# Kernel tuning notes

Hardware: AMD Instinct MI355X
Metric: run time of the kernel (lower is better)

The kernel has to match this reference:

```python
import jax, jax.numpy as jnp
import numpy as np

B, S, D = 2, 2048, 2048
H, KVH, HD = 16, 4, 128
GROUPS = H // KVH
SCALE = HD ** -0.5


def rotate_half(x):
    half = x.shape[-1] // 2
    return jnp.concatenate((-x[..., half:], x[..., :half]), axis=-1)


def apply_rope(q, k, cos, sin):
    # q,k: [B,S,H,HD]; cos,sin: [S,HD//2] -> repeat_interleave(2) -> [S,HD]
    cos = jnp.repeat(cos, 2, axis=-1)[None, :, None, :]
    sin = jnp.repeat(sin, 2, axis=-1)[None, :, None, :]
    return q * cos + rotate_half(q) * sin, k * cos + rotate_half(k) * sin


def setup_inputs() -> dict:
    key = jax.random.key(0)
    ks = jax.random.split(key, 8)
    inp = {
        'x': jax.random.normal(ks[0], (B, S, D), dtype=jnp.float32),
        'cos': jnp.cos(jnp.arange(S, dtype=jnp.float32)[:, None] * (1.0 / (10000.0 ** (jnp.arange(HD // 2, dtype=jnp.float32) / (HD // 2))))[None, :].reshape(1, HD // 2)),
        'sin': None,
        'mask': jnp.tril(jnp.ones((S, S), dtype=bool))[None, None, :, :],
        'Wq': jax.random.normal(ks[1], (D, H * HD), dtype=jnp.float32) * (D ** -0.5),
        'Wk': jax.random.normal(ks[2], (D, KVH * HD), dtype=jnp.float32) * (D ** -0.5),
        'Wv': jax.random.normal(ks[3], (D, KVH * HD), dtype=jnp.float32) * (D ** -0.5),
        'Wo': jax.random.normal(ks[4], (H * HD, D), dtype=jnp.float32) * ((H * HD) ** -0.5),
    }
    inv_freq = 1.0 / (10000.0 ** (jnp.arange(0, HD // 2, dtype=jnp.float32) / (HD // 2)))
    freqs = jnp.arange(S, dtype=jnp.float32)[:, None] * inv_freq[None, :]  # [S, HD//2]
    inp['cos'] = jnp.cos(freqs)
    inp['sin'] = jnp.sin(freqs)
    return inp


def reference(x, cos, sin, mask, Wq, Wk, Wv, Wo):
    b, s, _ = x.shape
    q = (x @ Wq).reshape(b, s, H, HD)    # [B,S,H,HD]
    k = (x @ Wk).reshape(b, s, KVH, HD)  # [B,S,KVH,HD]
    v = (x @ Wv).reshape(b, s, KVH, HD)
    q, k = apply_rope(q, k, cos, sin)
    q = q.transpose(0, 2, 1, 3)  # [B,H,S,HD]
    k = k.transpose(0, 2, 1, 3)  # [B,KVH,S,HD]
    v = v.transpose(0, 2, 1, 3)
    k = jnp.repeat(k, GROUPS, axis=1)  # [B,H,S,HD]
    v = jnp.repeat(v, GROUPS, axis=1)
    scores = jnp.einsum('bhqd,bhkd->bhqk', q, k) * SCALE
    scores = jnp.where(mask, scores, -jnp.inf)
    attn = jax.nn.softmax(scores, axis=-1)
    out = jnp.einsum('bhqk,bhkd->bhqd', attn, v)
    out = out.transpose(0, 2, 1, 3).reshape(b, s, H * HD)
    return out @ Wo
```

## Files before the change

kernel.cpp:

```cpp
#include <hip/hip_runtime.h>
#include <hip/hip_bf16.h>
#include <cstdint>
#include <type_traits>

typedef __attribute__((ext_vector_type(8))) short short8;
typedef __attribute__((ext_vector_type(4))) float floatx4;

constexpr int S_LEN = 2048;
constexpr float ATTN_SCALE = 0.08838834764831845f;
constexpr float LOG2E = 1.4426950408889634f;
constexpr float CP = ATTN_SCALE * LOG2E;

__device__ __forceinline__ void gl_lds16(const void* gp, void* lp) {
  __builtin_amdgcn_global_load_lds(
      (__attribute__((address_space(1))) void*)(uintptr_t)gp,
      (__attribute__((address_space(3))) void*)lp,
      16, 0, 0);
}

__device__ __forceinline__ float rowmax16(float x) {
  union { float f; int i; } a, b;
  a.f = x;
  b.i = __builtin_amdgcn_update_dpp(0, a.i, 0x121, 0xF, 0xF, true);
  x = fmaxf(x, b.f); a.f = x;
  b.i = __builtin_amdgcn_update_dpp(0, a.i, 0x122, 0xF, 0xF, true);
  x = fmaxf(x, b.f); a.f = x;
  b.i = __builtin_amdgcn_update_dpp(0, a.i, 0x124, 0xF, 0xF, true);
  x = fmaxf(x, b.f); a.f = x;
  b.i = __builtin_amdgcn_update_dpp(0, a.i, 0x128, 0xF, 0xF, true);
  return fmaxf(x, b.f);
}

__device__ __forceinline__ void rope8(short8 x0, short8 x1, const float* ca,
                                      const float* sa, const float* cb,
                                      const float* sb, short8& y0, short8& y1) {
#pragma unroll
  for (int e = 0; e < 8; ++e) {
    union { short s; __hip_bfloat16 h; } u0, u1, w0, w1;
    u0.s = x0[e]; u1.s = x1[e];
    float f0 = __bfloat162float(u0.h), f1 = __bfloat162float(u1.h);
    int j = e >> 1;
    w0.h = __float2bfloat16(f0 * ca[j] - f1 * sa[j]);
    w1.h = __float2bfloat16(f1 * cb[j] + f0 * sb[j]);
    y0[e] = w0.s; y1[e] = w1.s;
  }
}

__device__ __forceinline__ void tr32(const float* __restrict__ src,
                                     __hip_bfloat16* __restrict__ dst,
                                     int blk, int nblk_x, int N, int tid,
                                     float (*tile)[33]) {
  int n0 = (blk % nblk_x) * 32, k0 = (blk / nblk_x) * 32;
  int tx = tid & 31, ty = tid >> 5;
#pragma unroll
  for (int i = ty; i < 32; i += 8)
    tile[i][tx] = src[(size_t)(k0 + i) * N + n0 + tx];
  __syncthreads();
#pragma unroll
  for (int i = ty; i < 32; i += 8)
    dst[(size_t)(n0 + i) * 2048 + k0 + tx] = __float2bfloat16(tile[tx][i]);
}

__global__ void prep_kernel(const float* __restrict__ x,
                            const float* __restrict__ Wq,
                            const float* __restrict__ Wk,
                            const float* __restrict__ Wv,
                            const float* __restrict__ Wo,
                            __hip_bfloat16* __restrict__ xb,
                            __hip_bfloat16* __restrict__ wqkvt,
                            __hip_bfloat16* __restrict__ wot) {
  __shared__ float tile[32][33];
  int bx = blockIdx.x, tid = threadIdx.x;
  if (bx < 8192) {
    int i = bx * 256 + tid;
    float4 f = reinterpret_cast<const float4*>(x)[i];
    union { unsigned long long u64; __hip_bfloat16 h[4]; } u;
    u.h[0] = __float2bfloat16(f.x);
    u.h[1] = __float2bfloat16(f.y);
    u.h[2] = __float2bfloat16(f.z);
    u.h[3] = __float2bfloat16(f.w);
    reinterpret_cast<unsigned long long*>(xb)[i] = u.u64;
  } else if (bx < 12288) {
    tr32(Wq, wqkvt, bx - 8192, 64, 2048, tid, tile);
  } else if (bx < 13312) {
    tr32(Wk, wqkvt + 2048 * 2048, bx - 12288, 16, 512, tid, tile);
  } else if (bx < 14336) {
    tr32(Wv, wqkvt + 2560 * 2048, bx - 13312, 16, 512, tid, tile);
  } else {
    tr32(Wo, wot, bx - 14336, 64, 2048, tid, tile);
  }
}

__device__ __forceinline__ void gemm256_core(
    const __hip_bfloat16* __restrict__ Ab,
    const __hip_bfloat16* __restrict__ Bb,
    const int K, __hip_bfloat16* lds, floatx4 (&acc)[8][4]) {
  const int tid = threadIdx.x;
  const int wave = tid >> 6, lane = tid & 63;
  const int quad = lane >> 4, l15 = lane & 15;
  const int wm = wave >> 2, wn = wave & 3;
  const int nt = K >> 6;
  const int u2 = wave * 2;

  auto stA = [&](int tt, int h) {
    __hip_bfloat16* dst = lds + (tt & 1) * 32768;
    const int k0 = tt << 6;
#pragma unroll
    for (int j = 0; j < 2; ++j) {
      const int kc = (u2 + j) >> 1, rb = (u2 + j) & 1;
      gl_lds16(Ab + (size_t)(h * 128 + rb * 64 + lane) * K + k0 + kc * 8,
               dst + (kc * 256 + h * 128 + rb * 64) * 8);
    }
  };
  auto stB = [&](int tt, int h) {
    __hip_bfloat16* dst = lds + (tt & 1) * 32768 + 16384;
    const int k0 = tt << 6;
#pragma unroll
    for (int j = 0; j < 2; ++j) {
      const int kc = (u2 + j) >> 1, rb = (u2 + j) & 1;
      gl_lds16(Bb + (size_t)(h * 128 + rb * 64 + lane) * K + k0 + kc * 8,
               dst + (kc * 256 + h * 128 + rb * 64) * 8);
    }
  };

  stA(0, 0); stA(0, 1); stB(0, 0); stB(0, 1);
  if (nt > 1) { stB(1, 0); stB(1, 1); }
  asm volatile("s_waitcnt vmcnt(4)" ::: "memory");
  __builtin_amdgcn_s_barrier();

  const int abase = (quad * 256 + wm * 128 + l15) * 8;
  const int bbase = (quad * 256 + wn * 64 + l15) * 8;

#pragma unroll 2
  for (int t = 0; t < nt; ++t) {
    const __hip_bfloat16* Al = lds + (t & 1) * 32768;
    const __hip_bfloat16* Bl = Al + 16384;
    short8 b[2][4];
#pragma unroll
    for (int q = 0; q < 4; ++q) {
      short8 a[2][2];
#pragma unroll
      for (int kk = 0; kk < 2; ++kk) {
        if (q == 0) {
#pragma unroll
          for (int ni = 0; ni < 4; ++ni)
            b[kk][ni] = *(const short8*)&Bl[kk * 8192 + bbase + ni * 128];
        }
#pragma unroll
        for (int mi = 0; mi < 2; ++mi)
          a[kk][mi] = *(const short8*)&Al[kk * 8192 + abase + (2 * q + mi) * 128];
      }
      if (q == 0)      { if (t + 1 < nt) stA(t + 1, 0); }
      else if (q == 1) { if (t + 1 < nt) stA(t + 1, 1); }
      else if (q == 2) { if (t + 2 < nt) stB(t + 2, 0); }
      else             { if (t + 2 < nt) stB(t + 2, 1); }
      __builtin_amdgcn_s_barrier();
      asm volatile("s_waitcnt lgkmcnt(0)" ::: "memory");
      __builtin_amdgcn_sched_barrier(0);
      __builtin_amdgcn_s_setprio(1);
#pragma unroll
      for (int kk = 0; kk < 2; ++kk)
#pragma unroll
        for (int mi = 0; mi < 2; ++mi)
#pragma unroll
          for (int ni = 0; ni < 4; ++ni)
            acc[2 * q + mi][ni] = __builtin_amdgcn_mfma_f32_16x16x32_bf16(
                a[kk][mi], b[kk][ni], acc[2 * q + mi][ni], 0, 0, 0);
      __builtin_amdgcn_s_setprio(0);
      if (q == 3) {
        if (t + 2 < nt) asm volatile("s_waitcnt vmcnt(4)" ::: "memory");
        else            asm volatile("s_waitcnt vmcnt(0)" ::: "memory");
      }
      __builtin_amdgcn_s_barrier();
    }
  }
  asm volatile("" ::: "memory");
}

__global__ __launch_bounds__(512, 2) void qkv_gemm_kernel(
    const __hip_bfloat16* __restrict__ A,
    const __hip_bfloat16* __restrict__ Bt,
    __hip_bfloat16* __restrict__ qbuf,
    __hip_bfloat16* __restrict__ kbuf,
    __hip_bfloat16* __restrict__ vbuf,
    const float* __restrict__ cosb,
    const float* __restrict__ sinb) {
  constexpr int K = 2048;
  __shared__ __align__(16) __hip_bfloat16 lds[65536];
  const int tid = threadIdx.x;
  const int m0 = blockIdx.y * 256, n0 = blockIdx.x * 256;

  floatx4 acc[8][4] = {};
  gemm256_core(A + (size_t)m0 * K, Bt + (size_t)n0 * K, K, lds, acc);

  const int wave = tid >> 6, lane = tid & 63;
  const int quad = lane >> 4, l15 = lane & 15;
  const int wm = wave >> 2, wn = wave & 3;
  const bool isv = (n0 >= 2560);
  short* lds2 = (short*)lds;
#pragma unroll
  for (int mi = 0; mi < 8; ++mi)
#pragma unroll
    for (int ni = 0; ni < 4; ++ni)
#pragma unroll
      for (int r = 0; r < 4; ++r) {
        int row = wm * 128 + mi * 16 + quad * 4 + r;
        int col = wn * 64 + ni * 16 + l15;
        union { short s; __hip_bfloat16 h; } u;
        u.h = __float2bfloat16(acc[mi][ni][r]);
        if (isv) lds2[col * 256 + row] = u.s;
        else     lds2[row * 256 + col] = u.s;
      }
  __syncthreads();

  const int c16 = tid & 15, hh = c16 >> 3, c8 = c16 & 7;
  const int rid = tid >> 4, d0 = c8 * 8;
  if (n0 < 2048) {
#pragma unroll
    for (int j = 0; j < 8; ++j) {
      int rr = rid + 32 * j;
      int rowg = m0 + rr;
      int s = rowg & (S_LEN - 1);
      float ca[4], sa[4], cb[4], sb[4];
      *(float4*)ca = *(const float4*)&cosb[s * 64 + c8 * 4];
      *(float4*)sa = *(const float4*)&sinb[s * 64 + c8 * 4];
      *(float4*)cb = *(const float4*)&cosb[s * 64 + 32 + c8 * 4];
      *(float4*)sb = *(const float4*)&sinb[s * 64 + 32 + c8 * 4];
      short8 x0 = *(const short8*)&lds2[rr * 256 + hh * 128 + d0];
      short8 x1 = *(const short8*)&lds2[rr * 256 + hh * 128 + 64 + d0];
      short8 y0, y1;
      rope8(x0, x1, ca, sa, cb, sb, y0, y1);
      *(short8*)(qbuf + (size_t)rowg * 2048 + n0 + hh * 128 + d0) = y0;
      *(short8*)(qbuf + (size_t)rowg * 2048 + n0 + hh * 128 + 64 + d0) = y1;
    }
  } else if (!isv) {
    const int kvh = ((n0 - 2048) >> 7) + hh;
#pragma unroll
    for (int j = 0; j < 8; ++j) {
      int rr = rid + 32 * j;
      int rowg = m0 + rr;
      int s = rowg & (S_LEN - 1), bb = rowg >> 11;
      int kv = s & 63;
      size_t tb = ((size_t)(bb * 4 + kvh) * 32 + (s >> 6)) * 8192;
      float ca[4], sa[4], cb[4], sb[4];
      *(float4*)ca = *(const float4*)&cosb[s * 64 + c8 * 4];
      *(float4*)sa = *(const float4*)&sinb[s * 64 + c8 * 4];
      *(float4*)cb = *(const float4*)&cosb[s * 64 + 32 + c8 * 4];
      *(float4*)sb = *(const float4*)&sinb[s * 64 + 32 + c8 * 4];
      short8 x0 = *(const short8*)&lds2[rr * 256 + hh * 128 + d0];
      short8 x1 = *(const short8*)&lds2[rr * 256 + hh * 128 + 64 + d0];
      short8 y0, y1;
      rope8(x0, x1, ca, sa, cb, sb, y0, y1);
      *(short8*)(kbuf + tb + (size_t)c8 * 512 + kv * 8) = y0;
      *(short8*)(kbuf + tb + (size_t)(8 + c8) * 512 + kv * 8) = y1;
    }
  } else {
    const int kvh = ((n0 - 2560) >> 7) + hh;
    const int bb = m0 >> 11;
    const int kt0 = (m0 & (S_LEN - 1)) >> 6;
    const int kv0 = c8 * 8;
#pragma unroll
    for (int j = 0; j < 4; ++j) {
      int d = rid + 32 * j;
      int cxor = (d & 7) << 3;
#pragma unroll
      for (int half = 0; half < 4; ++half) {
        short8 vv = *(const short8*)&lds2[(hh * 128 + d) * 256 + half * 64 + kv0];
        size_t tb = ((size_t)(bb * 4 + kvh) * 32 + kt0 + half) * 8192;
        *(short8*)(vbuf + tb + d * 64 + (kv0 ^ cxor)) = vv;
      }
    }
  }
}

__global__ __launch_bounds__(512, 2) void gemm_bt_f32_kernel(
    const __hip_bfloat16* __restrict__ A,
    const __hip_bfloat16* __restrict__ Bt,
    float* __restrict__ C, int N, int K) {
  __shared__ __align__(16) __hip_bfloat16 lds[65536];
  const int tid = threadIdx.x;
  const int m0 = blockIdx.y * 256, n0 = blockIdx.x * 256;

  floatx4 acc[8][4] = {};
  gemm256_core(A + (size_t)m0 * K, Bt + (size_t)n0 * K, K, lds, acc);

  const int wave = tid >> 6, lane = tid & 63;
  const int quad = lane >> 4, l15 = lane & 15;
  const int wm = wave >> 2, wn = wave & 3;
#pragma unroll
  for (int mi = 0; mi < 8; ++mi)
#pragma unroll
    for (int ni = 0; ni < 4; ++ni)
#pragma unroll
      for (int r = 0; r < 4; ++r) {
        int row = m0 + wm * 128 + mi * 16 + quad * 4 + r;
        int col = n0 + wn * 64 + ni * 16 + l15;
        C[(size_t)row * N + col] = acc[mi][ni][r];
      }
}

__global__ __launch_bounds__(256, 2) void attn_kernel(
    const __hip_bfloat16* __restrict__ qbuf,
    const __hip_bfloat16* __restrict__ kbuf,
    const __hip_bfloat16* __restrict__ vbuf,
    __hip_bfloat16* __restrict__ aout) {
  const int qt = (blockIdx.y & 16) ? blockIdx.x : (15 - blockIdx.x);
  const int bh = blockIdx.y;
  const int b = bh >> 4, h = bh & 15;
  const int kvh = h >> 2;

  __shared__ __align__(16) __hip_bfloat16 Kbuf[2][8192];
  __shared__ __align__(16) __hip_bfloat16 Vbuf[2][8192];
  __shared__ __align__(16) __hip_bfloat16 Plds[4 * 16 * 72];

  const int tid = threadIdx.x;
  const int wave = tid >> 6, lane = tid & 63;
  const int quad = lane >> 4, l15 = lane & 15;

  short8 qfrag[2][4];
#pragma unroll
  for (int rs = 0; rs < 2; ++rs)
#pragma unroll
    for (int kc = 0; kc < 4; ++kc)
      qfrag[rs][kc] = *(const short8*)(qbuf +
          (size_t)(b * S_LEN + qt * 128 + rs * 64 + wave * 16 + l15) * 2048 +
          h * 128 + kc * 32 + quad * 8);

  const __hip_bfloat16* ktiles = kbuf + (size_t)(b * 4 + kvh) * 32 * 8192;
  const __hip_bfloat16* vtiles = vbuf + (size_t)(b * 4 + kvh) * 32 * 8192;
  const int nt = 2 * qt + 2;

#pragma unroll
  for (int j = 0; j < 4; ++j) {
    int c = tid + 256 * j;
    gl_lds16(ktiles + c * 8, &Kbuf[0][c * 8]);
    gl_lds16(vtiles + c * 8, &Vbuf[0][c * 8]);
  }

  float m_r[2][4];
  floatx4 o[2][8] = {};
  floatx4 o_l[2] = {};
#pragma unroll
  for (int rs = 0; rs < 2; ++rs)
#pragma unroll
    for (int r = 0; r < 4; ++r) m_r[rs][r] = -1e30f;

  short8 onesb;
#pragma unroll
  for (int e = 0; e < 8; ++e) onesb[e] = (short)0x3F80;

  __hip_bfloat16* pw = &Plds[wave * 16 * 72];

  for (int kt = 0; kt < nt; ++kt) {
    const int cur = kt & 1;
    __syncthreads();

    if (kt + 1 < nt) {
      const __hip_bfloat16* kb = ktiles + (size_t)(kt + 1) * 8192;
      const __hip_bfloat16* vb = vtiles + (size_t)(kt + 1) * 8192;
#pragma unroll
      for (int j = 0; j < 4; ++j) {
        int c = tid + 256 * j;
        gl_lds16(kb + c * 8, &Kbuf[1 - cur][c * 8]);
        gl_lds16(vb + c * 8, &Vbuf[1 - cur][c * 8]);
      }
    }

    floatx4 sc[2][4] = {};
#pragma unroll
    for (int ni = 0; ni < 4; ++ni)
#pragma unroll
      for (int kc = 0; kc < 4; ++kc) {
        short8 bf = *(const short8*)&Kbuf[cur][((kc * 4 + quad) * 64 + ni * 16 + l15) * 8];
        sc[0][ni] = __builtin_amdgcn_mfma_f32_16x16x32_bf16(qfrag[0][kc], bf, sc[0][ni], 0, 0, 0);
        sc[1][ni] = __builtin_amdgcn_mfma_f32_16x16x32_bf16(qfrag[1][kc], bf, sc[1][ni], 0, 0, 0);
      }

    short8 pa[2][2];
#pragma unroll
    for (int rs = 0; rs < 2; ++rs) {
      const int qt64 = 2 * qt + rs;
      if (kt >= qt64) {
        const int qrow = qt * 128 + rs * 64 + wave * 16 + quad * 4;
#pragma unroll
        for (int ni = 0; ni < 4; ++ni) {
          int kvcol = kt * 64 + ni * 16 + l15;
#pragma unroll
          for (int r = 0; r < 4; ++r)
            if (kvcol > qrow + r) sc[rs][ni][r] = -1e30f;
        }
      }

      float alpha[4];
#pragma unroll
      for (int r = 0; r < 4; ++r) {
        float v = fmaxf(fmaxf(sc[rs][0][r], sc[rs][1][r]),
                        fmaxf(sc[rs][2][r], sc[rs][3][r]));
        v = rowmax16(v);
        float mnew = fmaxf(m_r[rs][r], v);
        alpha[r] = exp2f((m_r[rs][r] - mnew) * CP);
        m_r[rs][r] = mnew;
        float mc = mnew * CP;
#pragma unroll
        for (int ni = 0; ni < 4; ++ni) {
          float p = exp2f(sc[rs][ni][r] * CP - mc);
          pw[(quad * 4 + r) * 72 + ni * 16 + l15] = __float2bfloat16(p);
        }
      }

#pragma unroll
      for (int kk2 = 0; kk2 < 2; ++kk2)
        pa[rs][kk2] = *(const short8*)&pw[l15 * 72 + kk2 * 32 + quad * 8];

#pragma unroll
      for (int nc = 0; nc < 8; ++nc)
#pragma unroll
        for (int r = 0; r < 4; ++r) o[rs][nc][r] *= alpha[r];
#pragma unroll
      for (int r = 0; r < 4; ++r) o_l[rs][r] *= alpha[r];
    }

#pragma unroll
    for (int kk2 = 0; kk2 < 2; ++kk2) {
#pragma unroll
      for (int nc = 0; nc < 8; ++nc) {
        int d = nc * 16 + l15;
        int swcol = (kk2 * 32 + quad * 8) ^ ((d & 7) << 3);
        short8 vv = *(const short8*)&Vbuf[cur][d * 64 + swcol];
        o[0][nc] = __builtin_amdgcn_mfma_f32_16x16x32_bf16(pa[0][kk2], vv, o[0][nc], 0, 0, 0);
        o[1][nc] = __builtin_amdgcn_mfma_f32_16x16x32_bf16(pa[1][kk2], vv, o[1][nc], 0, 0, 0);
      }
      o_l[0] = __builtin_amdgcn_mfma_f32_16x16x32_bf16(pa[0][kk2], onesb, o_l[0], 0, 0, 0);
      o_l[1] = __builtin_amdgcn_mfma_f32_16x16x32_bf16(pa[1][kk2], onesb, o_l[1], 0, 0, 0);
    }
  }

#pragma unroll
  for (int rs = 0; rs < 2; ++rs) {
    float inv[4];
#pragma unroll
    for (int r = 0; r < 4; ++r) inv[r] = 1.0f / o_l[rs][r];
    const size_t orow0 = (size_t)(b * S_LEN + qt * 128 + rs * 64 + wave * 16 + quad * 4);
#pragma unroll
    for (int nc = 0; nc < 8; ++nc)
#pragma unroll
      for (int r = 0; r < 4; ++r)
        aout[(orow0 + r) * 2048 + h * 128 + nc * 16 + l15] =
            __float2bfloat16(o[rs][nc][r] * inv[r]);
  }
}

extern "C" void kernel_launch(void* const* d_in, const int* in_sizes, int n_in,
                              void* d_out, int out_size, void* d_ws, size_t ws_size,
                              hipStream_t stream) {
  const float* x    = (const float*)d_in[0];
  const float* cosb = (const float*)d_in[1];
  const float* sinb = (const float*)d_in[2];
  const float* Wq = (const float*)d_in[4];
  const float* Wk = (const float*)d_in[5];
  const float* Wv = (const float*)d_in[6];
  const float* Wo = (const float*)d_in[7];
  float* out = (float*)d_out;

  char* ws = (char*)d_ws;
  __hip_bfloat16* xb    = (__hip_bfloat16*)(ws);
  __hip_bfloat16* wqkvt = (__hip_bfloat16*)(ws + (16u << 20));
  __hip_bfloat16* wot   = (__hip_bfloat16*)(ws + (28u << 20));
  __hip_bfloat16* qbuf  = (__hip_bfloat16*)(ws + (36u << 20));
  __hip_bfloat16* kbuf  = (__hip_bfloat16*)(ws + (52u << 20));
  __hip_bfloat16* vbuf  = (__hip_bfloat16*)(ws + (56u << 20));
  __hip_bfloat16* aout  = (__hip_bfloat16*)(ws + (60u << 20));

  prep_kernel<<<18432, 256, 0, stream>>>(x, Wq, Wk, Wv, Wo, xb, wqkvt, wot);
  qkv_gemm_kernel<<<dim3(12, 16), 512, 0, stream>>>(xb, wqkvt, qbuf, kbuf, vbuf, cosb, sinb);
  attn_kernel<<<dim3(16, 32), 256, 0, stream>>>(qbuf, kbuf, vbuf, aout);
  gemm_bt_f32_kernel<<<dim3(8, 16), 512, 0, stream>>>(aout, wot, out, 2048, 2048);
}
```

Before: 378.7 us.

## Use 256x128 tiles for output GEMM and register-resident P with lazy rescale in attention

The output projection GEMM moves to a new 256x128 tile core, doubling the grid from 128 to 256 blocks so more CUs are busy on a 2048x2048 output. The attention kernel computes S^T (operands swapped) so each lane holds a full query row. This replaces the LDS round-trip for P with cross-lane shuffles, drops the ones-vector MFMA in favour of a register row sum, and rescales O only when the row max grows past a threshold. The risks are extra shuffle overhead and the numerical approximation from the lazy-rescale threshold.

Result: faster. 366.7 us (-3.2%).

```diff
diff --git a/kernel.cpp b/kernel.cpp
--- a/kernel.cpp
+++ b/kernel.cpp
@@ -10,25 +10,13 @@
 constexpr float ATTN_SCALE = 0.08838834764831845f;
 constexpr float LOG2E = 1.4426950408889634f;
 constexpr float CP = ATTN_SCALE * LOG2E;
+constexpr float THRR = 5.0f / CP;
 
 __device__ __forceinline__ void gl_lds16(const void* gp, void* lp) {
   __builtin_amdgcn_global_load_lds(
       (__attribute__((address_space(1))) void*)(uintptr_t)gp,
       (__attribute__((address_space(3))) void*)lp,
       16, 0, 0);
-}
-
-__device__ __forceinline__ float rowmax16(float x) {
-  union { float f; int i; } a, b;
-  a.f = x;
-  b.i = __builtin_amdgcn_update_dpp(0, a.i, 0x121, 0xF, 0xF, true);
-  x = fmaxf(x, b.f); a.f = x;
-  b.i = __builtin_amdgcn_update_dpp(0, a.i, 0x122, 0xF, 0xF, true);
-  x = fmaxf(x, b.f); a.f = x;
-  b.i = __builtin_amdgcn_update_dpp(0, a.i, 0x124, 0xF, 0xF, true);
-  x = fmaxf(x, b.f); a.f = x;
-  b.i = __builtin_amdgcn_update_dpp(0, a.i, 0x128, 0xF, 0xF, true);
-  return fmaxf(x, b.f);
 }
 
 __device__ __forceinline__ void rope8(short8 x0, short8 x1, const float* ca,
@@ -177,6 +165,102 @@
   asm volatile("" ::: "memory");
 }
 
+__device__ __forceinline__ void gemm_256x128_core(
+    const __hip_bfloat16* __restrict__ Ab,
+    const __hip_bfloat16* __restrict__ Bb,
+    const int K, __hip_bfloat16* lds, floatx4 (&acc)[4][4]) {
+  const int tid = threadIdx.x;
+  const int wave = tid >> 6, lane = tid & 63;
+  const int quad = lane >> 4, l15 = lane & 15;
+  const int wm = wave >> 1, wn = wave & 1;
+  const int nt = K >> 6;
+
+  auto stA = [&](int tt, int c) {
+    __hip_bfloat16* dst = lds + (tt & 1) * 24576;
+    const int k0 = tt << 6;
+    const int i = c * 8 + wave;
+    const int kc = i >> 2, rb = i & 3;
+    gl_lds16(Ab + (size_t)(rb * 64 + lane) * K + k0 + kc * 8,
+             dst + (kc * 256 + rb * 64) * 8);
+  };
+  auto stB = [&](int tt, int c) {
+    __hip_bfloat16* dst = lds + (tt & 1) * 24576 + 16384;
+    const int k0 = tt << 6;
+    const int i = c * 8 + wave;
+    const int kc = i >> 1, rb = i & 1;
+    gl_lds16(Bb + (size_t)(rb * 64 + lane) * K + k0 + kc * 8,
+             dst + (kc * 128 + rb * 64) * 8);
+  };
+
+  stA(0, 0); stA(0, 1); stA(0, 2); stA(0, 3);
+  stB(0, 0); stB(0, 1);
+  if (nt > 1) {
+    stB(1, 0); stB(1, 1);
+    asm volatile("s_waitcnt vmcnt(2)" ::: "memory");
+  } else {
+    asm volatile("s_waitcnt vmcnt(0)" ::: "memory");
+  }
+  __builtin_amdgcn_s_barrier();
+
+  const int abase = (quad * 256 + wm * 64 + l15) * 8;
+  const int bbase = (quad * 128 + wn * 64 + l15) * 8;
+
+#pragma unroll 2
+  for (int t = 0; t < nt; ++t) {
+    const __hip_bfloat16* Al = lds + (t & 1) * 24576;
+    const __hip_bfloat16* Bl = Al + 16384;
+    short8 b[2][4], a[2][2];
+#pragma unroll
+    for (int kk = 0; kk < 2; ++kk) {
+#pragma unroll
+      for (int ni = 0; ni < 4; ++ni)
+        b[kk][ni] = *(const short8*)&Bl[kk * 4096 + bbase + ni * 128];
+#pragma unroll
+      for (int mi = 0; mi < 2; ++mi)
+        a[kk][mi] = *(const short8*)&Al[kk * 8192 + abase + mi * 128];
+    }
+    if (t + 1 < nt) { stA(t + 1, 0); stA(t + 1, 1); }
+    __builtin_amdgcn_s_barrier();
+    asm volatile("s_waitcnt lgkmcnt(0)" ::: "memory");
+    __builtin_amdgcn_sched_barrier(0);
+    __builtin_amdgcn_s_setprio(1);
+#pragma unroll
+    for (int kk = 0; kk < 2; ++kk)
+#pragma unroll
+      for (int mi = 0; mi < 2; ++mi)
+#pragma unroll
+        for (int ni = 0; ni < 4; ++ni)
+          acc[mi][ni] = __builtin_amdgcn_mfma_f32_16x16x32_bf16(
+              a[kk][mi], b[kk][ni], acc[mi][ni], 0, 0, 0);
+    __builtin_amdgcn_s_setprio(0);
+    __builtin_amdgcn_s_barrier();
+#pragma unroll
+    for (int kk = 0; kk < 2; ++kk)
+#pragma unroll
+      for (int mi = 0; mi < 2; ++mi)
+        a[kk][mi] = *(const short8*)&Al[kk * 8192 + abase + (2 + mi) * 128];
+    if (t + 1 < nt) { stA(t + 1, 2); stA(t + 1, 3); }
+    if (t + 2 < nt) { stB(t + 2, 0); stB(t + 2, 1); }
+    __builtin_amdgcn_s_barrier();
+    asm volatile("s_waitcnt lgkmcnt(0)" ::: "memory");
+    __builtin_amdgcn_sched_barrier(0);
+    __builtin_amdgcn_s_setprio(1);
+#pragma unroll
+    for (int kk = 0; kk < 2; ++kk)
+#pragma unroll
+      for (int mi = 0; mi < 2; ++mi)
+#pragma unroll
+        for (int ni = 0; ni < 4; ++ni)
+          acc[2 + mi][ni] = __builtin_amdgcn_mfma_f32_16x16x32_bf16(
+              a[kk][mi], b[kk][ni], acc[2 + mi][ni], 0, 0, 0);
+    __builtin_amdgcn_s_setprio(0);
+    if (t + 2 < nt) asm volatile("s_waitcnt vmcnt(2)" ::: "memory");
+    else            asm volatile("s_waitcnt vmcnt(0)" ::: "memory");
+    __builtin_amdgcn_s_barrier();
+  }
+  asm volatile("" ::: "memory");
+}
+
 __global__ __launch_bounds__(512, 2) void qkv_gemm_kernel(
     const __hip_bfloat16* __restrict__ A,
     const __hip_bfloat16* __restrict__ Bt,
@@ -277,23 +361,23 @@
     const __hip_bfloat16* __restrict__ A,
     const __hip_bfloat16* __restrict__ Bt,
     float* __restrict__ C, int N, int K) {
-  __shared__ __align__(16) __hip_bfloat16 lds[65536];
+  __shared__ __align__(16) __hip_bfloat16 lds[49152];
   const int tid = threadIdx.x;
-  const int m0 = blockIdx.y * 256, n0 = blockIdx.x * 256;
-
-  floatx4 acc[8][4] = {};
-  gemm256_core(A + (size_t)m0 * K, Bt + (size_t)n0 * K, K, lds, acc);
+  const int m0 = blockIdx.y * 256, n0 = blockIdx.x * 128;
+
+  floatx4 acc[4][4] = {};
+  gemm_256x128_core(A + (size_t)m0 * K, Bt + (size_t)n0 * K, K, lds, acc);
 
   const int wave = tid >> 6, lane = tid & 63;
   const int quad = lane >> 4, l15 = lane & 15;
-  const int wm = wave >> 2, wn = wave & 3;
-#pragma unroll
-  for (int mi = 0; mi < 8; ++mi)
+  const int wm = wave >> 1, wn = wave & 1;
+#pragma unroll
+  for (int mi = 0; mi < 4; ++mi)
 #pragma unroll
     for (int ni = 0; ni < 4; ++ni)
 #pragma unroll
       for (int r = 0; r < 4; ++r) {
-        int row = m0 + wm * 128 + mi * 16 + quad * 4 + r;
+        int row = m0 + wm * 64 + mi * 16 + quad * 4 + r;
         int col = n0 + wn * 64 + ni * 16 + l15;
         C[(size_t)row * N + col] = acc[mi][ni][r];
       }
@@ -311,7 +395,6 @@
 
   __shared__ __align__(16) __hip_bfloat16 Kbuf[2][8192];
   __shared__ __align__(16) __hip_bfloat16 Vbuf[2][8192];
-  __shared__ __align__(16) __hip_bfloat16 Plds[4 * 16 * 72];
 
   const int tid = threadIdx.x;
   const int wave = tid >> 6, lane = tid & 63;
@@ -337,19 +420,9 @@
     gl_lds16(vtiles + c * 8, &Vbuf[0][c * 8]);
   }
 
-  float m_r[2][4];
+  float m_s[2] = {-1e30f, -1e30f};
+  float l_s[2] = {0.f, 0.f};
   floatx4 o[2][8] = {};
-  floatx4 o_l[2] = {};
-#pragma unroll
-  for (int rs = 0; rs < 2; ++rs)
-#pragma unroll
-    for (int r = 0; r < 4; ++r) m_r[rs][r] = -1e30f;
-
-  short8 onesb;
-#pragma unroll
-  for (int e = 0; e < 8; ++e) onesb[e] = (short)0x3F80;
-
-  __hip_bfloat16* pw = &Plds[wave * 16 * 72];
 
   for (int kt = 0; kt < nt; ++kt) {
     const int cur = kt & 1;
@@ -372,8 +445,8 @@
 #pragma unroll
       for (int kc = 0; kc < 4; ++kc) {
         short8 bf = *(const short8*)&Kbuf[cur][((kc * 4 + quad) * 64 + ni * 16 + l15) * 8];
-        sc[0][ni] = __builtin_amdgcn_mfma_f32_16x16x32_bf16(qfrag[0][kc], bf, sc[0][ni], 0, 0, 0);
-        sc[1][ni] = __builtin_amdgcn_mfma_f32_16x16x32_bf16(qfrag[1][kc], bf, sc[1][ni], 0, 0, 0);
+        sc[0][ni] = __builtin_amdgcn_mfma_f32_16x16x32_bf16(bf, qfrag[0][kc], sc[0][ni], 0, 0, 0);
+        sc[1][ni] = __builtin_amdgcn_mfma_f32_16x16x32_bf16(bf, qfrag[1][kc], sc[1][ni], 0, 0, 0);
       }
 
     short8 pa[2][2];
@@ -381,43 +454,72 @@
     for (int rs = 0; rs < 2; ++rs) {
       const int qt64 = 2 * qt + rs;
       if (kt >= qt64) {
-        const int qrow = qt * 128 + rs * 64 + wave * 16 + quad * 4;
+        const int qg = qt * 128 + rs * 64 + wave * 16 + l15;
 #pragma unroll
         for (int ni = 0; ni < 4; ++ni) {
-          int kvcol = kt * 64 + ni * 16 + l15;
+          int kvb = kt * 64 + ni * 16 + quad * 4;
 #pragma unroll
           for (int r = 0; r < 4; ++r)
-            if (kvcol > qrow + r) sc[rs][ni][r] = -1e30f;
+            if (kvb + r > qg) sc[rs][ni][r] = -1e30f;
         }
       }
 
-      float alpha[4];
-#pragma unroll
-      for (int r = 0; r < 4; ++r) {
-        float v = fmaxf(fmaxf(sc[rs][0][r], sc[rs][1][r]),
-                        fmaxf(sc[rs][2][r], sc[rs][3][r]));
-        v = rowmax16(v);
-        float mnew = fmaxf(m_r[rs][r], v);
-        alpha[r] = exp2f((m_r[rs][r] - mnew) * CP);
-        m_r[rs][r] = mnew;
-        float mc = mnew * CP;
-#pragma unroll
-        for (int ni = 0; ni < 4; ++ni) {
-          float p = exp2f(sc[rs][ni][r] * CP - mc);
-          pw[(quad * 4 + r) * 72 + ni * 16 + l15] = __float2bfloat16(p);
+      float v = sc[rs][0][0];
+#pragma unroll
+      for (int ni = 0; ni < 4; ++ni)
+#pragma unroll
+        for (int r = 0; r < 4; ++r) v = fmaxf(v, sc[rs][ni][r]);
+      v = fmaxf(v, __shfl_xor(v, 16));
+      v = fmaxf(v, __shfl_xor(v, 32));
+
+      float mold = m_s[rs];
+      if (__any(v > mold + THRR)) {
+        float mnew = fmaxf(mold, v);
+        float alpha = exp2f((mold - mnew) * CP);
+        m_s[rs] = mnew;
+        l_s[rs] *= alpha;
+        float ar[4];
+#pragma unroll
+        for (int r = 0; r < 4; ++r)
+          ar[r] = __shfl(alpha, (lane & 48) + quad * 4 + r);
+#pragma unroll
+        for (int nc = 0; nc < 8; ++nc)
+#pragma unroll
+          for (int r = 0; r < 4; ++r) o[rs][nc][r] *= ar[r];
+      }
+
+      float mc = m_s[rs] * CP;
+      unsigned pk[4][2];
+      float lsum = 0.f;
+#pragma unroll
+      for (int ni = 0; ni < 4; ++ni)
+#pragma unroll
+        for (int pr = 0; pr < 2; ++pr) {
+          float p0 = exp2f(sc[rs][ni][2 * pr] * CP - mc);
+          float p1 = exp2f(sc[rs][ni][2 * pr + 1] * CP - mc);
+          lsum += p0 + p1;
+          union { unsigned u; ushort us[2]; } uu;
+          union { __hip_bfloat16 h; ushort us; } b0, b1;
+          b0.h = __float2bfloat16(p0); b1.h = __float2bfloat16(p1);
+          uu.us[0] = b0.us; uu.us[1] = b1.us;
+          pk[ni][pr] = uu.u;
         }
-      }
-
-#pragma unroll
-      for (int kk2 = 0; kk2 < 2; ++kk2)
-        pa[rs][kk2] = *(const short8*)&pw[l15 * 72 + kk2 * 32 + quad * 8];
-
-#pragma unroll
-      for (int nc = 0; nc < 8; ++nc)
-#pragma unroll
-        for (int r = 0; r < 4; ++r) o[rs][nc][r] *= alpha[r];
-#pragma unroll
-      for (int r = 0; r < 4; ++r) o_l[rs][r] *= alpha[r];
+      lsum += __shfl_xor(lsum, 16);
+      lsum += __shfl_xor(lsum, 32);
+      l_s[rs] += lsum;
+
+#pragma unroll
+      for (int kk2 = 0; kk2 < 2; ++kk2) {
+        union { unsigned w[4]; short8 s; } pw_;
+#pragma unroll
+        for (int j = 0; j < 4; ++j) {
+          int src = ((((quad & 1) * 2) + (j >> 1)) << 4) | l15;
+          unsigned lo = (unsigned)__shfl((int)pk[2 * kk2][j & 1], src);
+          unsigned hi = (unsigned)__shfl((int)pk[2 * kk2 + 1][j & 1], src);
+          pw_.w[j] = (quad >> 1) ? hi : lo;
+        }
+        pa[rs][kk2] = pw_.s;
+      }
     }
 
 #pragma unroll
@@ -430,8 +532,6 @@
         o[0][nc] = __builtin_amdgcn_mfma_f32_16x16x32_bf16(pa[0][kk2], vv, o[0][nc], 0, 0, 0);
         o[1][nc] = __builtin_amdgcn_mfma_f32_16x16x32_bf16(pa[1][kk2], vv, o[1][nc], 0, 0, 0);
       }
-      o_l[0] = __builtin_amdgcn_mfma_f32_16x16x32_bf16(pa[0][kk2], onesb, o_l[0], 0, 0, 0);
-      o_l[1] = __builtin_amdgcn_mfma_f32_16x16x32_bf16(pa[1][kk2], onesb, o_l[1], 0, 0, 0);
     }
   }
 
@@ -439,7 +539,10 @@
   for (int rs = 0; rs < 2; ++rs) {
     float inv[4];
 #pragma unroll
-    for (int r = 0; r < 4; ++r) inv[r] = 1.0f / o_l[rs][r];
+    for (int r = 0; r < 4; ++r) {
+      float lr = __shfl(l_s[rs], (lane & 48) + quad * 4 + r);
+      inv[r] = 1.0f / lr;
+    }
     const size_t orow0 = (size_t)(b * S_LEN + qt * 128 + rs * 64 + wave * 16 + quad * 4);
 #pragma unroll
     for (int nc = 0; nc < 8; ++nc)
@@ -474,5 +577,5 @@
   prep_kernel<<<18432, 256, 0, stream>>>(x, Wq, Wk, Wv, Wo, xb, wqkvt, wot);
   qkv_gemm_kernel<<<dim3(12, 16), 512, 0, stream>>>(xb, wqkvt, qbuf, kbuf, vbuf, cosb, sinb);
   attn_kernel<<<dim3(16, 32), 256, 0, stream>>>(qbuf, kbuf, vbuf, aout);
-  gemm_bt_f32_kernel<<<dim3(8, 16), 512, 0, stream>>>(aout, wot, out, 2048, 2048);
-}
+  gemm_bt_f32_kernel<<<dim3(16, 16), 512, 0, stream>>>(aout, wot, out, 2048, 2048);
+}
```
